# Kernel optimization log

Hardware: AMD Instinct MI355X
Metric: run time of the kernel (lower is better)

The kernel has to match this reference:

```python
import jax, jax.numpy as jnp
import numpy as np
from jax import lax

BATCH = 8192
NUM_REFS = 2048
DIM = 256
REF_CHUNK = 64  # stream R in chunks to avoid a [B, R, dim] intermediate


def setup_inputs() -> dict:
    key = jax.random.key(0)
    k1, k2 = jax.random.split(key)
    # bit-like states/reference set (Ising / hamming-style energy)
    states = jnp.round(jax.random.uniform(k1, (BATCH, DIM), dtype=jnp.float32))
    R = jnp.round(jax.random.uniform(k2, (NUM_REFS, DIM), dtype=jnp.float32))
    return {"states": states, "R": R}


def reference(states, R):
    # states: [B, dim] (original flattens higher-rank batch dims to this form)
    # R:      [num_refs, dim]
    # out:    [B] = min_r sum_d |states[b,d] - R[r,d]|
    states = states.astype(jnp.float32)
    B, dim = states.shape
    num_refs = R.shape[0]
    R_chunks = R.reshape(num_refs // REF_CHUNK, REF_CHUNK, dim)

    def step(running_min, r_chunk):
        # [B, chunk, dim] -> [B, chunk] -> [B]; chunked so peak temp is small
        d = jnp.abs(states[:, None, :] - r_chunk[None, :, :]).sum(-1).min(1)
        return jnp.minimum(running_min, d), None

    init = jnp.full((B,), jnp.inf, dtype=states.dtype)
    out, _ = lax.scan(step, init, R_chunks)
    return out
```

## Files before the change

kernel.cpp:

```cpp
#include <hip/hip_runtime.h>
#include <stdint.h>

#define BATCH 8192
#define NREF  2048
#define DIM   256

#define WORDS64 (DIM / 64)
#define S_WORDS (BATCH * WORDS64)
#define R_WORDS (NREF * WORDS64)
#define TOT_WORDS (S_WORDS + R_WORDS)

#define CHUNK  64
#define NCHUNK (NREF / CHUNK)
#define TPB    256
#define BPT    2
#define BPB    (TPB * BPT)
#define NBBLK  (BATCH / BPB)

__global__ void pack_kernel(const float* __restrict__ states,
                            const float* __restrict__ R,
                            unsigned long long* __restrict__ sp,
                            unsigned long long* __restrict__ rp) {
    const int lane = threadIdx.x & 63;
    int gw = (blockIdx.x * blockDim.x + threadIdx.x) >> 6;
    const int nw = (gridDim.x * blockDim.x) >> 6;
    for (int w = gw; w < TOT_WORDS; w += nw) {
        const float* src;
        unsigned long long* dst;
        int idx;
        if (w < S_WORDS) { src = states; dst = sp; idx = w; }
        else             { src = R;      dst = rp; idx = w - S_WORDS; }
        const float f = src[(size_t)idx * 64 + lane];
        const unsigned long long m = __ballot(f > 0.5f);
        if (lane == 0) dst[idx] = m;
    }
}

__global__ __launch_bounds__(TPB) void hamming_kernel(
        const uint4* __restrict__ sp,
        const uint4* __restrict__ rp,
        int* __restrict__ partial) {
    __shared__ uint4 lds[CHUNK * 2];

    const int chunk = blockIdx.x;
    const int bblk  = blockIdx.y;
    const int t     = threadIdx.x;

    if (t < CHUNK * 2) lds[t] = rp[chunk * (CHUNK * 2) + t];
    __syncthreads();

    const int b0 = bblk * BPB + t;
    const int b1 = b0 + TPB;

    const uint4 sa0 = sp[2 * b0], sa1 = sp[2 * b0 + 1];
    const uint4 sb0 = sp[2 * b1], sb1 = sp[2 * b1 + 1];

    int m0 = 0x7fffffff, m1 = 0x7fffffff;

#pragma unroll 8
    for (int r = 0; r < CHUNK; ++r) {
        const uint4 r0 = lds[2 * r];
        const uint4 r1 = lds[2 * r + 1];
        int h0 = __popc(r0.x ^ sa0.x) + __popc(r0.y ^ sa0.y)
               + __popc(r0.z ^ sa0.z) + __popc(r0.w ^ sa0.w)
               + __popc(r1.x ^ sa1.x) + __popc(r1.y ^ sa1.y)
               + __popc(r1.z ^ sa1.z) + __popc(r1.w ^ sa1.w);
        int h1 = __popc(r0.x ^ sb0.x) + __popc(r0.y ^ sb0.y)
               + __popc(r0.z ^ sb0.z) + __popc(r0.w ^ sb0.w)
               + __popc(r1.x ^ sb1.x) + __popc(r1.y ^ sb1.y)
               + __popc(r1.z ^ sb1.z) + __popc(r1.w ^ sb1.w);
        m0 = min(m0, h0);
        m1 = min(m1, h1);
    }

    partial[chunk * BATCH + b0] = m0;
    partial[chunk * BATCH + b1] = m1;
}

__global__ void reduce_kernel(const int* __restrict__ partial,
                              float* __restrict__ out) {
    const int b = blockIdx.x * blockDim.x + threadIdx.x;
    int m = partial[b];
#pragma unroll
    for (int c = 1; c < NCHUNK; ++c) m = min(m, partial[c * BATCH + b]);
    out[b] = (float)m;
}

extern "C" void kernel_launch(void* const* d_in, const int* in_sizes, int n_in,
                              void* d_out, int out_size, void* d_ws, size_t ws_size,
                              hipStream_t stream) {
    const float* states = (const float*)d_in[0];
    const float* R      = (const float*)d_in[1];
    float* out          = (float*)d_out;

    char* ws = (char*)d_ws;
    unsigned long long* sp64 = (unsigned long long*)ws;
    unsigned long long* rp64 = (unsigned long long*)(ws + 262144);
    int* partial             = (int*)(ws + 262144 + 65536);

    pack_kernel<<<640, 256, 0, stream>>>(states, R, sp64, rp64);

    dim3 grid(NCHUNK, NBBLK);
    hamming_kernel<<<grid, TPB, 0, stream>>>((const uint4*)sp64,
                                             (const uint4*)rp64, partial);

    reduce_kernel<<<BATCH / 256, 256, 0, stream>>>(partial, out);
}
```

Before: 78.58 us.

## Replace partial-min buffer and reduce kernel with atomicMin, repack bits per byte

Result: faster. 69.20 us (-11.9%).

```diff
diff --git a/kernel.cpp b/kernel.cpp
--- a/kernel.cpp
+++ b/kernel.cpp
@@ -5,10 +5,9 @@
 #define NREF  2048
 #define DIM   256
 
-#define WORDS64 (DIM / 64)
-#define S_WORDS (BATCH * WORDS64)
-#define R_WORDS (NREF * WORDS64)
-#define TOT_WORDS (S_WORDS + R_WORDS)
+#define SBYTES (BATCH * 32)
+#define RBYTES (NREF * 32)
+#define TOTB   (SBYTES + RBYTES)
 
 #define CHUNK  64
 #define NCHUNK (NREF / CHUNK)
@@ -17,29 +16,40 @@
 #define BPB    (TPB * BPT)
 #define NBBLK  (BATCH / BPB)
 
-__global__ void pack_kernel(const float* __restrict__ states,
-                            const float* __restrict__ R,
-                            unsigned long long* __restrict__ sp,
-                            unsigned long long* __restrict__ rp) {
-    const int lane = threadIdx.x & 63;
-    int gw = (blockIdx.x * blockDim.x + threadIdx.x) >> 6;
-    const int nw = (gridDim.x * blockDim.x) >> 6;
-    for (int w = gw; w < TOT_WORDS; w += nw) {
-        const float* src;
-        unsigned long long* dst;
-        int idx;
-        if (w < S_WORDS) { src = states; dst = sp; idx = w; }
-        else             { src = R;      dst = rp; idx = w - S_WORDS; }
-        const float f = src[(size_t)idx * 64 + lane];
-        const unsigned long long m = __ballot(f > 0.5f);
-        if (lane == 0) dst[idx] = m;
-    }
+__global__ __launch_bounds__(256) void pack_init_kernel(
+        const float* __restrict__ states,
+        const float* __restrict__ R,
+        uint8_t* __restrict__ sp,
+        uint8_t* __restrict__ rp,
+        float* __restrict__ out) {
+    const int gid = blockIdx.x * blockDim.x + threadIdx.x;
+
+    if (gid < BATCH) out[gid] = __int_as_float(0x7f800000);
+
+    const float4* src;
+    uint8_t* dst;
+    int idx;
+    if (gid < SBYTES) { src = (const float4*)states; dst = sp; idx = gid; }
+    else              { src = (const float4*)R;      dst = rp; idx = gid - SBYTES; }
+
+    const float4 v0 = src[idx * 2];
+    const float4 v1 = src[idx * 2 + 1];
+    unsigned int b = 0;
+    b |= (v0.x > 0.5f) ? 0x01u : 0u;
+    b |= (v0.y > 0.5f) ? 0x02u : 0u;
+    b |= (v0.z > 0.5f) ? 0x04u : 0u;
+    b |= (v0.w > 0.5f) ? 0x08u : 0u;
+    b |= (v1.x > 0.5f) ? 0x10u : 0u;
+    b |= (v1.y > 0.5f) ? 0x20u : 0u;
+    b |= (v1.z > 0.5f) ? 0x40u : 0u;
+    b |= (v1.w > 0.5f) ? 0x80u : 0u;
+    dst[idx] = (uint8_t)b;
 }
 
 __global__ __launch_bounds__(TPB) void hamming_kernel(
         const uint4* __restrict__ sp,
         const uint4* __restrict__ rp,
-        int* __restrict__ partial) {
+        float* __restrict__ out) {
     __shared__ uint4 lds[CHUNK * 2];
 
     const int chunk = blockIdx.x;
@@ -73,17 +83,8 @@
         m1 = min(m1, h1);
     }
 
-    partial[chunk * BATCH + b0] = m0;
-    partial[chunk * BATCH + b1] = m1;
-}
-
-__global__ void reduce_kernel(const int* __restrict__ partial,
-                              float* __restrict__ out) {
-    const int b = blockIdx.x * blockDim.x + threadIdx.x;
-    int m = partial[b];
-#pragma unroll
-    for (int c = 1; c < NCHUNK; ++c) m = min(m, partial[c * BATCH + b]);
-    out[b] = (float)m;
+    atomicMin((int*)&out[b0], __float_as_int((float)m0));
+    atomicMin((int*)&out[b1], __float_as_int((float)m1));
 }
 
 extern "C" void kernel_launch(void* const* d_in, const int* in_sizes, int n_in,
@@ -94,15 +95,12 @@
     float* out          = (float*)d_out;
 
     char* ws = (char*)d_ws;
-    unsigned long long* sp64 = (unsigned long long*)ws;
-    unsigned long long* rp64 = (unsigned long long*)(ws + 262144);
-    int* partial             = (int*)(ws + 262144 + 65536);
+    uint8_t* sp = (uint8_t*)ws;
+    uint8_t* rp = (uint8_t*)(ws + SBYTES);
 
-    pack_kernel<<<640, 256, 0, stream>>>(states, R, sp64, rp64);
+    pack_init_kernel<<<TOTB / 256, 256, 0, stream>>>(states, R, sp, rp, out);
 
     dim3 grid(NCHUNK, NBBLK);
-    hamming_kernel<<<grid, TPB, 0, stream>>>((const uint4*)sp64,
-                                             (const uint4*)rp64, partial);
-
-    reduce_kernel<<<BATCH / 256, 256, 0, stream>>>(partial, out);
+    hamming_kernel<<<grid, TPB, 0, stream>>>((const uint4*)sp,
+                                             (const uint4*)rp, out);
 }
```
